# Optimization experiments

Hardware: AMD Instinct MI355X
Metric: run time of the kernel (lower is better)

Reference implementation:

```python
import jax, jax.numpy as jnp
import numpy as np

B, S, E, H = 4, 2048, 1024, 16
K = 9           # number of boundaries per batch (K-1 = 8 passages)
DH = E // H


def make_relevance_mask(boundaries, relevance_scores, seq_len):
    """Vectorized equivalent of the Python-loop mask builder.

    boundaries: (B, K) int, sorted; boundaries[:,0] == q_end.
    relevance_scores: (B, K-1) float.
    Returns float mask (B, S, S) with values {0, 1, relevance}.
    """
    Bsz, Kb = boundaries.shape
    idx = jnp.arange(seq_len, dtype=boundaries.dtype)
    # pid[b, s] = j s.t. boundaries[b, j] <= s < boundaries[b, j+1]; -1 before b[0]
    pid = jax.vmap(lambda bb: jnp.searchsorted(bb, idx, side='right'))(boundaries) - 1  # (B,S)
    in_pass = (pid >= 0) & (pid < Kb - 1)  # inside some passage span
    rel_g = jnp.take_along_axis(relevance_scores, jnp.clip(pid, 0, Kb - 2), axis=1)  # (B,S)
    # query rows (pos < q_end): columns in passage j -> relevance[j], else 1
    col_val = jnp.where(in_pass, rel_g, 1.0)  # (B,S)
    qrow = idx[None, :] < boundaries[:, :1]   # (B,S)
    # non-query rows: 1 iff same passage block, else 0
    same = in_pass[:, :, None] & in_pass[:, None, :] & (pid[:, :, None] == pid[:, None, :])
    mask = jnp.where(qrow[:, :, None], col_val[:, None, :], jnp.where(same, 1.0, 0.0))
    return mask.astype(jnp.float32)


def setup_inputs() -> dict:
    key = jax.random.key(0)
    k1, k2, k3, k4, k5, k6, k7 = jax.random.split(key, 7)
    hidden_states = jax.random.normal(k1, (B, S, E), dtype=jnp.float32)
    relevance_scores = jax.random.uniform(k2, (B, K - 1), dtype=jnp.float32)
    passage_boundaries = jnp.sort(jax.random.randint(k3, (B, K), 0, S, dtype=jnp.int32), axis=1)
    in_proj_w = 0.02 * jax.random.normal(k4, (3 * E, E), dtype=jnp.float32)
    in_proj_b = jnp.zeros((3 * E,), dtype=jnp.float32)
    out_w = 0.02 * jax.random.normal(k5, (E, E), dtype=jnp.float32)
    out_b = jnp.zeros((E,), dtype=jnp.float32)
    return {
        'hidden_states': hidden_states,
        'relevance_scores': relevance_scores,
        'passage_boundaries': passage_boundaries,
        'in_proj_w': in_proj_w,
        'in_proj_b': in_proj_b,
        'out_w': out_w,
        'out_b': out_b,
    }


def reference(hidden_states, relevance_scores, passage_boundaries,
              in_proj_w, in_proj_b, out_w, out_b):
    Bsz, Sl, Em = hidden_states.shape
    mask = make_relevance_mask(passage_boundaries, relevance_scores, Sl)  # (B,S,S)
    qkv = hidden_states @ in_proj_w.T + in_proj_b              # (B,S,3E)
    q, k, v = jnp.split(qkv, 3, axis=-1)
    def heads(t):
        return t.reshape(Bsz, Sl, H, DH).transpose(0, 2, 1, 3)  # (B,H,S,Dh)
    q, k, v = heads(q), heads(k), heads(v)
    scale = 1.0 / jnp.sqrt(jnp.float32(DH))
    scores = jnp.einsum('bhqd,bhkd->bhqk', q * scale, k) + mask[:, None]  # float mask is ADDED
    attn = jax.nn.softmax(scores, axis=-1)
    out = jnp.einsum('bhqk,bhkd->bhqd', attn, v)
    out = out.transpose(0, 2, 1, 3).reshape(Bsz, Sl, Em)
    return out @ out_w.T + out_b
```

## Files before the change

kernel.cpp:

```cpp
#include <hip/hip_runtime.h>
#include <math.h>

#define Bsz 4
#define Sq  2048
#define Eq  1024
#define Hh  16
#define DHd 64
#define Kb  9
#define LOG2E 1.44269504088896340736f
#define NCLS 10

typedef _Float16 f16;
typedef __attribute__((ext_vector_type(8))) _Float16 fh8;
typedef __attribute__((ext_vector_type(4))) _Float16 fh4;
typedef __attribute__((ext_vector_type(2))) _Float16 fh2;
typedef __attribute__((ext_vector_type(4))) float fx4;
typedef __attribute__((ext_vector_type(16))) float fx16;
typedef __attribute__((ext_vector_type(4))) int i4;

#define SWZ(r, c) ((r) * 64 + ((c) ^ (((r) & 7) << 3)))

static __device__ __forceinline__ float fexp2(float x) {
#if __has_builtin(__builtin_amdgcn_exp2f)
  return __builtin_amdgcn_exp2f(x);
#else
  return __expf(x * 0.6931471805599453f);
#endif
}

__global__ void pid_kernel(const int* __restrict__ bnd, const float* __restrict__ rel,
                           int* __restrict__ pidr, float* __restrict__ lfTab) {
  int idx = blockIdx.x * blockDim.x + threadIdx.x;
  if (idx >= Bsz * Sq) return;
  int b = idx >> 11;
  int s = idx & (Sq - 1);
  int j = -1;
#pragma unroll
  for (int t = 0; t < Kb; ++t) {
    if (bnd[b * Kb + t] <= s) j = t;
  }
  pidr[idx] = j;
  bool inp = (j >= 0 && j < Kb - 1);
  float cv = inp ? rel[b * (Kb - 1) + j] : 1.0f;
  float* base = &lfTab[(size_t)b * NCLS * Sq + s];
  base[0] = cv * LOG2E;
#pragma unroll
  for (int c = 1; c < NCLS; ++c)
    base[c * Sq] = (inp && j == c - 1) ? LOG2E : 0.0f;
}

__global__ __launch_bounds__(256) void cvt_hs(const float* __restrict__ x,
                                              f16* __restrict__ xo) {
  int i = (blockIdx.x * blockDim.x + threadIdx.x) * 8;
  float4 a = *(const float4*)&x[i];
  float4 b = *(const float4*)&x[i + 4];
  fh8 o;
  o[0] = (f16)a.x; o[1] = (f16)a.y; o[2] = (f16)a.z; o[3] = (f16)a.w;
  o[4] = (f16)b.x; o[5] = (f16)b.y; o[6] = (f16)b.z; o[7] = (f16)b.w;
  *(fh8*)&xo[i] = o;
}

template <int MODE>
__global__ __launch_bounds__(256) void gemm_f16(
    const f16* __restrict__ A, const f16* __restrict__ Bh,
    const float* __restrict__ bias, float* __restrict__ Cp,
    int M, int N, int Kd,
    f16* __restrict__ qo, f16* __restrict__ ko, f16* __restrict__ vto) {
  __shared__ __align__(16) f16 Ash[128 * 64];
  __shared__ __align__(16) f16 Bsh[128 * 64];

  const int tid = threadIdx.x;
  const int lane = tid & 63, w = tid >> 6;
  const int wm = w >> 1, wn = w & 1;
  const int q16 = lane & 15, quad = lane >> 4;
  const int m_blk = blockIdx.y * 128, n_blk = blockIdx.x * 128;

  fx4 acc[4][4];
#pragma unroll
  for (int mt = 0; mt < 4; ++mt)
#pragma unroll
    for (int nt = 0; nt < 4; ++nt)
#pragma unroll
      for (int r = 0; r < 4; ++r) acc[mt][nt][r] = 0.f;

  const int sr = tid >> 2, sc = (tid & 3) * 16;

  fh8 pa[2][2], pb[2][2];
  const f16* ga0 = &A[(size_t)(m_blk + sr) * Kd + sc];
  const f16* gb0 = &Bh[(size_t)(n_blk + sr) * Kd + sc];

#pragma unroll
  for (int h = 0; h < 2; ++h) {
    const f16* ga = ga0 + (size_t)h * 64 * Kd;
    pa[h][0] = *(const fh8*)&ga[0];
    pa[h][1] = *(const fh8*)&ga[8];
    const f16* gb = gb0 + (size_t)h * 64 * Kd;
    pb[h][0] = *(const fh8*)&gb[0];
    pb[h][1] = *(const fh8*)&gb[8];
  }

  for (int k0 = 0; k0 < Kd; k0 += 64) {
    __syncthreads();
#pragma unroll
    for (int h = 0; h < 2; ++h) {
      const int r = sr + h * 64;
      *(fh8*)&Ash[SWZ(r, sc)]     = pa[h][0];
      *(fh8*)&Ash[SWZ(r, sc + 8)] = pa[h][1];
      *(fh8*)&Bsh[SWZ(r, sc)]     = pb[h][0];
      *(fh8*)&Bsh[SWZ(r, sc + 8)] = pb[h][1];
    }
    if (k0 + 64 < Kd) {
      const int kn = k0 + 64;
#pragma unroll
      for (int h = 0; h < 2; ++h) {
        const f16* ga = ga0 + (size_t)h * 64 * Kd + kn;
        pa[h][0] = *(const fh8*)&ga[0];
        pa[h][1] = *(const fh8*)&ga[8];
        const f16* gb = gb0 + (size_t)h * 64 * Kd + kn;
        pb[h][0] = *(const fh8*)&gb[0];
        pb[h][1] = *(const fh8*)&gb[8];
      }
    }
    __syncthreads();

#pragma unroll
    for (int ks = 0; ks < 2; ++ks) {
      fh8 af[4], bfr[4];
#pragma unroll
      for (int mt = 0; mt < 4; ++mt)
        af[mt] = *(const fh8*)&Ash[SWZ(wm * 64 + mt * 16 + q16, ks * 32 + quad * 8)];
#pragma unroll
      for (int nt = 0; nt < 4; ++nt)
        bfr[nt] = *(const fh8*)&Bsh[SWZ(wn * 64 + nt * 16 + q16, ks * 32 + quad * 8)];
#pragma unroll
      for (int nt = 0; nt < 4; ++nt)
#pragma unroll
        for (int mt = 0; mt < 4; ++mt)
          acc[mt][nt] = __builtin_amdgcn_mfma_f32_16x16x32_f16(af[mt], bfr[nt], acc[mt][nt], 0, 0, 0);
    }
  }

  float bsv[4];
#pragma unroll
  for (int nt = 0; nt < 4; ++nt) bsv[nt] = bias[n_blk + wn * 64 + nt * 16 + q16];

  if (MODE == 0) {
#pragma unroll
    for (int mt = 0; mt < 4; ++mt)
#pragma unroll
      for (int r = 0; r < 4; ++r) {
        int row = m_blk + wm * 64 + mt * 16 + quad * 4 + r;
#pragma unroll
        for (int nt = 0; nt < 4; ++nt) {
          int col = n_blk + wn * 64 + nt * 16 + q16;
          Cp[(size_t)row * N + col] = acc[mt][nt][r] + bsv[nt];
        }
      }
  } else {
    const int n0 = n_blk + wn * 64;
    const int which = n0 >> 10;
    const int hd = (n0 & 1023) >> 6;
    const float scale = (which == 0) ? 0.125f * LOG2E : 1.0f;
#pragma unroll
    for (int mt = 0; mt < 4; ++mt)
#pragma unroll
      for (int r = 0; r < 4; ++r) {
        int m = m_blk + wm * 64 + mt * 16 + quad * 4 + r;
        int b = m >> 11, s = m & (Sq - 1);
#pragma unroll
        for (int nt = 0; nt < 4; ++nt) {
          int d = nt * 16 + q16;
          float x = (acc[mt][nt][r] + bsv[nt]) * scale;
          if (which == 2) {
            vto[(((size_t)(b * Hh + hd)) * DHd + d) * Sq + s] = (f16)x;
          } else {
            f16* dst = (which == 0) ? qo : ko;
            dst[(((size_t)(b * Hh + hd)) * Sq + s) * DHd + d] = (f16)x;
          }
        }
      }
  }
}

__global__ __launch_bounds__(256, 2) void attn_v6(
    const f16* __restrict__ Qf, const f16* __restrict__ Kf,
    const f16* __restrict__ Vt, const int* __restrict__ pidr,
    const float* __restrict__ lfTab, f16* __restrict__ attf) {
  const int lin = blockIdx.x;
  const int orig = (lin & 7) * 128 + (lin >> 3);
  const int qb = orig & 15, hd = (orig >> 4) & 15, b = orig >> 8;
  const int bh = b * Hh + hd;
  const int tid = threadIdx.x;
  const int lane = tid & 63, w = tid >> 6;
  const int l31 = lane & 31, hi = lane >> 5;

  __shared__ __align__(16) f16 Ks[2][64 * 64];
  __shared__ __align__(16) f16 Vs[2][64 * 64];

  const size_t qkbase = (size_t)bh * Sq * DHd;
  const size_t vtbase = (size_t)bh * DHd * Sq;
  const int qrow = qb * 128 + w * 32 + l31;

  fh8 qf[4];
  {
    const f16* qp = &Qf[qkbase + (size_t)qrow * DHd + hi * 8];
#pragma unroll
    for (int ds = 0; ds < 4; ++ds) qf[ds] = *(const fh8*)&qp[ds * 16];
  }

  const int rq = pidr[b * Sq + qrow];
  const float* lfrow = &lfTab[((size_t)(b * NCLS + (rq + 1))) * Sq + 4 * hi];

  fh8 onesf;
#pragma unroll
  for (int j = 0; j < 8; ++j) onesf[j] = (l31 == 0) ? (f16)1.0f : (f16)0.0f;

  fx16 o_acc[2], lacc;
#pragma unroll
  for (int r = 0; r < 16; ++r) { o_acc[0][r] = 0.f; o_acc[1][r] = 0.f; lacc[r] = 0.f; }

  const int sr = tid >> 2, sc = (tid & 3) * 16;
  const int NT = Sq / 64;

  fh8 kc0, kc1, vc0, vc1;
  {
    const f16* gk = &Kf[qkbase + (size_t)sr * DHd + sc];
    kc0 = *(const fh8*)&gk[0]; kc1 = *(const fh8*)&gk[8];
    const f16* gv = &Vt[vtbase + (size_t)sr * Sq + sc];
    vc0 = *(const fh8*)&gv[0]; vc1 = *(const fh8*)&gv[8];
  }
  *(fh8*)&Ks[0][SWZ(sr, sc)]     = kc0;
  *(fh8*)&Ks[0][SWZ(sr, sc + 8)] = kc1;
  *(fh8*)&Vs[0][SWZ(sr, sc)]     = vc0;
  *(fh8*)&Vs[0][SWZ(sr, sc + 8)] = vc1;
  {
    const f16* gk = &Kf[qkbase + (size_t)(64 + sr) * DHd + sc];
    kc0 = *(const fh8*)&gk[0]; kc1 = *(const fh8*)&gk[8];
    const f16* gv = &Vt[vtbase + (size_t)sr * Sq + 64 + sc];
    vc0 = *(const fh8*)&gv[0]; vc1 = *(const fh8*)&gv[8];
  }
  __syncthreads();

  fx16 sacc0, sacc1;

  for (int kt = 0; kt < NT; ++kt) {
    const int c = kt & 1;

    {
      const float* lp = &lfrow[kt * 64];
#pragma unroll
      for (int g = 0; g < 4; ++g) {
        float4 a = *(const float4*)&lp[8 * g];
        sacc0[4 * g + 0] = a.x; sacc0[4 * g + 1] = a.y;
        sacc0[4 * g + 2] = a.z; sacc0[4 * g + 3] = a.w;
      }
    }

    if (kt + 1 < NT) {
      *(fh8*)&Ks[c ^ 1][SWZ(sr, sc)]     = kc0;
      *(fh8*)&Ks[c ^ 1][SWZ(sr, sc + 8)] = kc1;
      *(fh8*)&Vs[c ^ 1][SWZ(sr, sc)]     = vc0;
      *(fh8*)&Vs[c ^ 1][SWZ(sr, sc + 8)] = vc1;
      if (kt + 2 < NT) {
        const f16* gk = &Kf[qkbase + (size_t)((kt + 2) * 64 + sr) * DHd + sc];
        kc0 = *(const fh8*)&gk[0]; kc1 = *(const fh8*)&gk[8];
        const f16* gv = &Vt[vtbase + (size_t)sr * Sq + (kt + 2) * 64 + sc];
        vc0 = *(const fh8*)&gv[0]; vc1 = *(const fh8*)&gv[8];
      }
    }

    auto half = [&](fx16& sacc, int s, bool preload_next) {
      fh8 kfr[4];
#pragma unroll
      for (int ds = 0; ds < 4; ++ds)
        kfr[ds] = *(const fh8*)&Ks[c][SWZ(s * 32 + l31, ds * 16 + hi * 8)];
      __builtin_amdgcn_s_setprio(1);
#pragma unroll
      for (int ds = 0; ds < 4; ++ds)
        sacc = __builtin_amdgcn_mfma_f32_32x32x16_f16(kfr[ds], qf[ds], sacc, 0, 0, 0);
      __builtin_amdgcn_s_setprio(0);

      if (preload_next) {
        const float* lp = &lfrow[kt * 64 + 32];
#pragma unroll
        for (int g = 0; g < 4; ++g) {
          float4 a = *(const float4*)&lp[8 * g];
          sacc1[4 * g + 0] = a.x; sacc1[4 * g + 1] = a.y;
          sacc1[4 * g + 2] = a.z; sacc1[4 * g + 3] = a.w;
        }
      }

      int pk[8];
#pragma unroll
      for (int i = 0; i < 8; ++i) {
        fh2 h;
        h[0] = (f16)fexp2(sacc[2 * i]);
        h[1] = (f16)fexp2(sacc[2 * i + 1]);
        pk[i] = __builtin_bit_cast(int, h);
      }

      fh8 vfr[2][2];
#pragma unroll
      for (int dt = 0; dt < 2; ++dt)
#pragma unroll
        for (int kb = 0; kb < 2; ++kb)
          vfr[dt][kb] = *(const fh8*)&Vs[c][SWZ(dt * 32 + l31, s * 32 + kb * 16 + hi * 8)];

      __builtin_amdgcn_s_setprio(1);
#pragma unroll
      for (int kb = 0; kb < 2; ++kb) {
        int a01 = pk[4 * kb + 0], a23 = pk[4 * kb + 1];
        int a45 = pk[4 * kb + 2], a67 = pk[4 * kb + 3];
        i4 t;
#if __has_builtin(__builtin_amdgcn_permlane32_swap)
        auto s0 = __builtin_amdgcn_permlane32_swap(a01, a45, false, false);
        auto s1 = __builtin_amdgcn_permlane32_swap(a23, a67, false, false);
        t[0] = s0[0]; t[1] = s1[0]; t[2] = s0[1]; t[3] = s1[1];
#else
        int x01 = __shfl_xor(a01, 32), x23 = __shfl_xor(a23, 32);
        int x45 = __shfl_xor(a45, 32), x67 = __shfl_xor(a67, 32);
        t[0] = hi ? x45 : a01; t[1] = hi ? x67 : a23;
        t[2] = hi ? a45 : x01; t[3] = hi ? a67 : x23;
#endif
        fh8 pf = __builtin_bit_cast(fh8, t);
        lacc = __builtin_amdgcn_mfma_f32_32x32x16_f16(onesf, pf, lacc, 0, 0, 0);
        o_acc[0] = __builtin_amdgcn_mfma_f32_32x32x16_f16(vfr[0][kb], pf, o_acc[0], 0, 0, 0);
        o_acc[1] = __builtin_amdgcn_mfma_f32_32x32x16_f16(vfr[1][kb], pf, o_acc[1], 0, 0, 0);
      }
      __builtin_amdgcn_s_setprio(0);
    };

    half(sacc0, 0, true);
    half(sacc1, 1, false);

    if (kt + 1 < NT) __syncthreads();
  }

  float l = __shfl(lacc[0], l31);
  float inv = 1.0f / l;
  size_t obase = ((size_t)(b * Sq + qrow)) * Eq + hd * 64 + 4 * hi;
#pragma unroll
  for (int dt = 0; dt < 2; ++dt)
#pragma unroll
    for (int g = 0; g < 4; ++g) {
      fh4 o4;
#pragma unroll
      for (int j = 0; j < 4; ++j) o4[j] = (f16)(o_acc[dt][4 * g + j] * inv);
      *(fh4*)&attf[obase + dt * 32 + 8 * g] = o4;
    }
}

extern "C" void kernel_launch(void* const* d_in, const int* in_sizes, int n_in,
                              void* d_out, int out_size, void* d_ws, size_t ws_size,
                              hipStream_t stream) {
  const float* hs = (const float*)d_in[0];
  const float* rel = (const float*)d_in[1];
  const int* bnd = (const int*)d_in[2];
  const float* wi = (const float*)d_in[3];
  const float* bi = (const float*)d_in[4];
  const float* wo = (const float*)d_in[5];
  const float* bo = (const float*)d_in[6];
  float* out = (float*)d_out;

  const size_t NQ = (size_t)Bsz * Hh * Sq * DHd;
  char* p = (char*)d_ws;
  f16* qf = (f16*)p;   p += NQ * 2;
  f16* kf = (f16*)p;   p += NQ * 2;
  f16* vt = (f16*)p;   p += NQ * 2;
  f16* hsf = (f16*)p;  p += NQ * 2;
  f16* attf = (f16*)p; p += NQ * 2;
  f16* wif = (f16*)p;  p += (size_t)3 * Eq * Eq * 2;
  f16* wof = (f16*)p;  p += (size_t)Eq * Eq * 2;
  int* pidr = (int*)p; p += Bsz * Sq * 4;
  float* lfTab = (float*)p;

  hipLaunchKernelGGL(pid_kernel, dim3((Bsz * Sq + 255) / 256), dim3(256), 0, stream,
                     bnd, rel, pidr, lfTab);
  hipLaunchKernelGGL(cvt_hs, dim3((int)(NQ / 2048)), dim3(256), 0, stream, hs, hsf);
  hipLaunchKernelGGL(cvt_hs, dim3(3 * Eq * Eq / 2048), dim3(256), 0, stream, wi, wif);
  hipLaunchKernelGGL(cvt_hs, dim3(Eq * Eq / 2048), dim3(256), 0, stream, wo, wof);
  hipLaunchKernelGGL((gemm_f16<1>), dim3(24, 64), dim3(256), 0, stream,
                     hsf, wif, bi, (float*)nullptr, Bsz * Sq, 3 * Eq, Eq,
                     qf, kf, vt);
  hipLaunchKernelGGL(attn_v6, dim3(16 * 16 * 4), dim3(256), 0, stream,
                     qf, kf, vt, pidr, lfTab, attf);
  hipLaunchKernelGGL((gemm_f16<0>), dim3(8, 64), dim3(256), 0, stream,
                     attf, wof, bo, out, Bsz * Sq, Eq, Eq,
                     nullptr, nullptr, nullptr);
}
```

Measured before the change: 301.8 us.

## Fuse conversions, XCD-aware GEMM tiling, scalar softmax row sum in attention

Merges the three fp32-to-fp16 conversion launches into one kernel, cutting launch overhead. Remaps GEMM block indices so each XCD works on a contiguous band of N columns, aiming for better L2 reuse of B tiles. In attention, the row-sum MFMA against a ones vector is replaced by a per-lane scalar sum of the fp16 probabilities combined with a lane-xor shuffle, and launch bounds are raised to 3 blocks per CU for occupancy. The scalar sum adds VALU work and register pressure may cause spills under the tighter launch bound.

```diff
diff --git a/kernel.cpp b/kernel.cpp
--- a/kernel.cpp
+++ b/kernel.cpp
@@ -49,18 +49,27 @@
     base[c * Sq] = (inp && j == c - 1) ? LOG2E : 0.0f;
 }
 
-__global__ __launch_bounds__(256) void cvt_hs(const float* __restrict__ x,
-                                              f16* __restrict__ xo) {
-  int i = (blockIdx.x * blockDim.x + threadIdx.x) * 8;
-  float4 a = *(const float4*)&x[i];
-  float4 b = *(const float4*)&x[i + 4];
+__global__ __launch_bounds__(256) void cvt_all(
+    const float* __restrict__ hs, f16* __restrict__ hsf,
+    const float* __restrict__ wi, f16* __restrict__ wif,
+    const float* __restrict__ wo, f16* __restrict__ wof) {
+  int bid = blockIdx.x;
+  const float* src;
+  f16* dst;
+  int off;
+  if (bid < 4096)      { src = hs; dst = hsf; off = bid; }
+  else if (bid < 5632) { src = wi; dst = wif; off = bid - 4096; }
+  else                 { src = wo; dst = wof; off = bid - 5632; }
+  int i = (off * 256 + threadIdx.x) * 8;
+  float4 a = *(const float4*)&src[i];
+  float4 b = *(const float4*)&src[i + 4];
   fh8 o;
   o[0] = (f16)a.x; o[1] = (f16)a.y; o[2] = (f16)a.z; o[3] = (f16)a.w;
   o[4] = (f16)b.x; o[5] = (f16)b.y; o[6] = (f16)b.z; o[7] = (f16)b.w;
-  *(fh8*)&xo[i] = o;
-}
-
-template <int MODE>
+  *(fh8*)&dst[i] = o;
+}
+
+template <int MODE, int NPX>
 __global__ __launch_bounds__(256) void gemm_f16(
     const f16* __restrict__ A, const f16* __restrict__ Bh,
     const float* __restrict__ bias, float* __restrict__ Cp,
@@ -73,7 +82,10 @@
   const int lane = tid & 63, w = tid >> 6;
   const int wm = w >> 1, wn = w & 1;
   const int q16 = lane & 15, quad = lane >> 4;
-  const int m_blk = blockIdx.y * 128, n_blk = blockIdx.x * 128;
+  const int lin = blockIdx.x;
+  const int xcd = lin & 7, i = lin >> 3;
+  const int n_blk = (xcd * NPX + (i % NPX)) * 128;
+  const int m_blk = (i / NPX) * 128;
 
   fx4 acc[4][4];
 #pragma unroll
@@ -182,7 +194,7 @@
   }
 }
 
-__global__ __launch_bounds__(256, 2) void attn_v6(
+__global__ __launch_bounds__(256, 3) void attn_v7(
     const f16* __restrict__ Qf, const f16* __restrict__ Kf,
     const f16* __restrict__ Vt, const int* __restrict__ pidr,
     const float* __restrict__ lfTab, f16* __restrict__ attf) {
@@ -211,13 +223,10 @@
   const int rq = pidr[b * Sq + qrow];
   const float* lfrow = &lfTab[((size_t)(b * NCLS + (rq + 1))) * Sq + 4 * hi];
 
-  fh8 onesf;
-#pragma unroll
-  for (int j = 0; j < 8; ++j) onesf[j] = (l31 == 0) ? (f16)1.0f : (f16)0.0f;
-
-  fx16 o_acc[2], lacc;
-#pragma unroll
-  for (int r = 0; r < 16; ++r) { o_acc[0][r] = 0.f; o_acc[1][r] = 0.f; lacc[r] = 0.f; }
+  fx16 o_acc[2];
+#pragma unroll
+  for (int r = 0; r < 16; ++r) { o_acc[0][r] = 0.f; o_acc[1][r] = 0.f; }
+  float lsum = 0.f;
 
   const int sr = tid >> 2, sc = (tid & 3) * 16;
   const int NT = Sq / 64;
@@ -296,6 +305,7 @@
         fh2 h;
         h[0] = (f16)fexp2(sacc[2 * i]);
         h[1] = (f16)fexp2(sacc[2 * i + 1]);
+        lsum += (float)h[0] + (float)h[1];
         pk[i] = __builtin_bit_cast(int, h);
       }
 
@@ -323,7 +333,6 @@
         t[2] = hi ? a45 : x01; t[3] = hi ? a67 : x23;
 #endif
         fh8 pf = __builtin_bit_cast(fh8, t);
-        lacc = __builtin_amdgcn_mfma_f32_32x32x16_f16(onesf, pf, lacc, 0, 0, 0);
         o_acc[0] = __builtin_amdgcn_mfma_f32_32x32x16_f16(vfr[0][kb], pf, o_acc[0], 0, 0, 0);
         o_acc[1] = __builtin_amdgcn_mfma_f32_32x32x16_f16(vfr[1][kb], pf, o_acc[1], 0, 0, 0);
       }
@@ -336,7 +345,7 @@
     if (kt + 1 < NT) __syncthreads();
   }
 
-  float l = __shfl(lacc[0], l31);
+  float l = lsum + __shfl_xor(lsum, 32);
   float inv = 1.0f / l;
   size_t obase = ((size_t)(b * Sq + qrow)) * Eq + hd * 64 + 4 * hi;
 #pragma unroll
@@ -376,15 +385,14 @@
 
   hipLaunchKernelGGL(pid_kernel, dim3((Bsz * Sq + 255) / 256), dim3(256), 0, stream,
                      bnd, rel, pidr, lfTab);
-  hipLaunchKernelGGL(cvt_hs, dim3((int)(NQ / 2048)), dim3(256), 0, stream, hs, hsf);
-  hipLaunchKernelGGL(cvt_hs, dim3(3 * Eq * Eq / 2048), dim3(256), 0, stream, wi, wif);
-  hipLaunchKernelGGL(cvt_hs, dim3(Eq * Eq / 2048), dim3(256), 0, stream, wo, wof);
-  hipLaunchKernelGGL((gemm_f16<1>), dim3(24, 64), dim3(256), 0, stream,
+  hipLaunchKernelGGL(cvt_all, dim3(6144), dim3(256), 0, stream,
+                     hs, hsf, wi, wif, wo, wof);
+  hipLaunchKernelGGL((gemm_f16<1, 3>), dim3(1536), dim3(256), 0, stream,
                      hsf, wif, bi, (float*)nullptr, Bsz * Sq, 3 * Eq, Eq,
                      qf, kf, vt);
-  hipLaunchKernelGGL(attn_v6, dim3(16 * 16 * 4), dim3(256), 0, stream,
+  hipLaunchKernelGGL(attn_v7, dim3(16 * 16 * 4), dim3(256), 0, stream,
                      qf, kf, vt, pidr, lfTab, attf);
-  hipLaunchKernelGGL((gemm_f16<0>), dim3(8, 64), dim3(256), 0, stream,
+  hipLaunchKernelGGL((gemm_f16<0, 1>), dim3(512), dim3(256), 0, stream,
                      attf, wof, bo, out, Bsz * Sq, Eq, Eq,
                      nullptr, nullptr, nullptr);
 }
```

After: 313.6 us. 3.9% more time.
